# Kernel tuning notes

Hardware: AMD Instinct MI355X
Metric: run time of the kernel (lower is better)

The kernel has to match this reference:

```python
import jax, jax.numpy as jnp
import numpy as np

# Static per-expert capacities (tokens are laid out contiguously per expert)
CAPS = [1024, 512, 1024, 256, 1024, 512, 128, 1024, 512, 1024, 256, 512, 1024, 128, 64, 512]
TOTAL = sum(CAPS)  # 9536
E, H, I = 16, 1024, 4096
OFFSETS = np.concatenate([[0], np.cumsum(CAPS)])


def setup_inputs() -> dict:
    key = jax.random.key(0)
    ks = jax.random.split(key, 5)
    x = jax.random.normal(ks[0], (TOTAL, H), dtype=jnp.float32)
    W1 = jax.random.normal(ks[1], (E, I, H), dtype=jnp.float32) * 0.02
    b1 = jax.random.normal(ks[2], (E, I), dtype=jnp.float32) * 0.02
    W2 = jax.random.normal(ks[3], (E, H, I), dtype=jnp.float32) * 0.02
    b2 = jax.random.normal(ks[4], (E, H), dtype=jnp.float32) * 0.02
    return {"x": x, "W1": W1, "b1": b1, "W2": W2, "b2": b2}


def reference(x, W1, b1, W2, b2):
    # Grouped GEMM FFN: expert e processes rows [OFFSETS[e]:OFFSETS[e+1]]
    # out = gelu(x_e @ W1[e].T + b1[e]) @ W2[e].T + b2[e]
    outs = []
    for e in range(E):  # fixed, static loop over experts (capacities are static)
        xs = x[OFFSETS[e]:OFFSETS[e + 1]]                      # [cap_e, H]
        h = jax.nn.gelu(xs @ W1[e].T + b1[e], approximate=False)  # [cap_e, I]
        outs.append(h @ W2[e].T + b2[e])                       # [cap_e, H]
    return jnp.concatenate(outs, axis=0)                       # [TOTAL, H]
```

## Files before the change

kernel.cpp:

```cpp
#include <hip/hip_runtime.h>
#include <math.h>

typedef __attribute__((ext_vector_type(8))) short short8;
typedef __attribute__((ext_vector_type(4))) float f32x4;
typedef __attribute__((ext_vector_type(2))) unsigned int u32x2;

#define E_NUM 16
constexpr int CAPS[E_NUM] = {1024,512,1024,256,1024,512,128,1024,512,1024,256,512,1024,128,64,512};
constexpr int OFFS[E_NUM] = {0,1024,1536,2560,2816,3840,4352,4480,5504,6016,7040,7296,7808,8832,8960,9024};
constexpr int cdiv_(int a, int b){ return (a + b - 1) / b; }
constexpr int ilog2_(int v){ int l = 0; while ((1 << l) < v) ++l; return l; }

__device__ __forceinline__ unsigned int cvt_pk_bf16(float a, float b){
  unsigned int r;
  asm("v_cvt_pk_bf16_f32 %0, %1, %2" : "=v"(r) : "v"(a), "v"(b));
  return r;
}

template<bool A_BF16, bool GELU_OUT, int TM, int NDIM, int KDIM, int LOG_GN, int NWG>
__global__ __launch_bounds__(256, 4)
void expert_gemm(const void* __restrict__ Av, const float* __restrict__ W,
                 const float* __restrict__ bias, void* __restrict__ Outv)
{
  constexpr int STR  = 40;
  constexpr int A_SZ = TM * STR;
  constexpr int B_SZ = 128 * STR;
  constexpr int GN   = 1 << LOG_GN;
  constexpr int MFR  = TM / 32;
  static_assert(NWG % 8 == 0, "grid must be divisible by 8 for XCD swizzle");

  __shared__ __align__(16) unsigned short smem[2 * A_SZ + 2 * B_SZ];

  const int tid  = threadIdx.x;
  const int braw = blockIdx.x;
  const int t = (braw & 7) * (NWG / 8) + (braw >> 3);

  int m0 = 0, n0 = 0, Me = 0, tok0 = 0;
  size_t wbase = 0, bbase = 0;
  {
    int acc0 = 0;
    #pragma unroll
    for (int i = 0; i < E_NUM; ++i) {
      const int mt  = cdiv_(CAPS[i], TM);
      const int lmt = ilog2_(mt);
      const int nb  = mt * (NDIM / 128);
      if (t >= acc0 && t < acc0 + nb) {
        const int loc = t - acc0;
        const int g   = loc >> (lmt + LOG_GN);
        const int rem = loc & ((mt << LOG_GN) - 1);
        m0   = (rem >> LOG_GN) * TM;
        n0   = ((g << LOG_GN) | (rem & (GN - 1))) * 128;
        Me   = CAPS[i];
        tok0 = OFFS[i];
        wbase = (size_t)i * NDIM * KDIM;
        bbase = (size_t)i * NDIM;
      }
      acc0 += nb;
    }
  }
  const float* Wb = W + wbase;

  const int sr  = tid >> 3;
  const int skq = (tid & 7) * 4;
  const int hr  = tid >> 2;
  const int hc  = (tid & 3) * 8;

  const float*          Af = (const float*)Av;
  const unsigned short* Ah = (const unsigned short*)Av;

  f32x4 ra[4]; short8 ha[2]; f32x4 rb[4];

  auto load_tile = [&](int kt) {
    const int k0 = kt * 32;
    if constexpr (A_BF16) {
      #pragma unroll
      for (int i = 0; i < TM / 64; ++i)
        ha[i] = *reinterpret_cast<const short8*>(
            Ah + (size_t)(tok0 + m0 + hr + 64 * i) * KDIM + k0 + hc);
    } else {
      #pragma unroll
      for (int i = 0; i < TM / 32; ++i)
        ra[i] = *reinterpret_cast<const f32x4*>(
            Af + (size_t)(tok0 + m0 + sr + 32 * i) * KDIM + k0 + skq);
    }
    #pragma unroll
    for (int i = 0; i < 4; ++i)
      rb[i] = *reinterpret_cast<const f32x4*>(
          Wb + (size_t)(n0 + sr + 32 * i) * KDIM + k0 + skq);
  };

  auto write_tile = [&](int buf) {
    unsigned short* ab = smem + buf * A_SZ;
    unsigned short* bb = smem + 2 * A_SZ + buf * B_SZ;
    if constexpr (A_BF16) {
      #pragma unroll
      for (int i = 0; i < TM / 64; ++i)
        *reinterpret_cast<short8*>(ab + (hr + 64 * i) * STR + hc) = ha[i];
    } else {
      #pragma unroll
      for (int i = 0; i < TM / 32; ++i) {
        u32x2 p;
        p[0] = cvt_pk_bf16(ra[i][0], ra[i][1]);
        p[1] = cvt_pk_bf16(ra[i][2], ra[i][3]);
        *reinterpret_cast<u32x2*>(ab + (sr + 32 * i) * STR + skq) = p;
      }
    }
    #pragma unroll
    for (int i = 0; i < 4; ++i) {
      u32x2 p;
      p[0] = cvt_pk_bf16(rb[i][0], rb[i][1]);
      p[1] = cvt_pk_bf16(rb[i][2], rb[i][3]);
      *reinterpret_cast<u32x2*>(bb + (sr + 32 * i) * STR + skq) = p;
    }
  };

  const int lane = tid & 63;
  const int wv   = tid >> 6;
  const int wm   = (wv >> 1) * (TM / 2);
  const int wn   = (wv & 1) * 64;
  const int lrow = lane & 15;
  const int kcol = (lane >> 4) * 8;

  f32x4 acc_[MFR][4];
  #pragma unroll
  for (int i = 0; i < MFR; ++i)
    #pragma unroll
    for (int j = 0; j < 4; ++j)
      acc_[i][j] = (f32x4){0.f, 0.f, 0.f, 0.f};

  load_tile(0);
  write_tile(0);
  __syncthreads();

  constexpr int NT = KDIM / 32;
  for (int kt = 0; kt < NT; ++kt) {
    const int cur = kt & 1;
    if (kt + 1 < NT) load_tile(kt + 1);

    const unsigned short* ab = smem + cur * A_SZ;
    const unsigned short* bb = smem + 2 * A_SZ + cur * B_SZ;
    short8 afr[MFR], bfr[4];
    #pragma unroll
    for (int f = 0; f < MFR; ++f)
      afr[f] = *reinterpret_cast<const short8*>(ab + (wm + f * 16 + lrow) * STR + kcol);
    #pragma unroll
    for (int f = 0; f < 4; ++f)
      bfr[f] = *reinterpret_cast<const short8*>(bb + (wn + f * 16 + lrow) * STR + kcol);

    #pragma unroll
    for (int i = 0; i < MFR; ++i)
      #pragma unroll
      for (int j = 0; j < 4; ++j)
        acc_[i][j] = __builtin_amdgcn_mfma_f32_16x16x32_bf16(afr[i], bfr[j], acc_[i][j], 0, 0, 0);

    if (kt + 1 < NT) write_tile(cur ^ 1);
    __syncthreads();
  }

  float bv[4];
  #pragma unroll
  for (int f = 0; f < 4; ++f)
    bv[f] = bias[bbase + n0 + wn + f * 16 + lrow];

  if constexpr (GELU_OUT) {
    static_assert(TM == 128, "GELU path assumes 128-row tiles");
    unsigned short* hout = smem;
    #pragma unroll
    for (int i = 0; i < MFR; ++i) {
      const int rbase = wm + i * 16 + (lane >> 4) * 4;
      #pragma unroll
      for (int j = 0; j < 4; ++j) {
        #pragma unroll
        for (int jj = 0; jj < 4; ++jj) {
          float xv = acc_[i][j][jj] + bv[j];
          float g  = 0.5f * xv * (1.0f + erff(xv * 0.70710678118654752f));
          hout[(rbase + jj) * 128 + wn + j * 16 + lrow] = (unsigned short)(cvt_pk_bf16(g, g) & 0xFFFFu);
        }
      }
    }
    __syncthreads();
    unsigned short* Oh = (unsigned short*)Outv;
    #pragma unroll
    for (int it = 0; it < 8; ++it) {
      int row  = it * 16 + (tid >> 4);
      int c    = (tid & 15) * 8;
      int grow = m0 + row;
      if (grow < Me) {
        *reinterpret_cast<short8*>(Oh + (size_t)(tok0 + grow) * NDIM + n0 + c)
          = *reinterpret_cast<const short8*>(hout + row * 128 + c);
      }
    }
  } else {
    float* Of = (float*)Outv;
    #pragma unroll
    for (int i = 0; i < MFR; ++i) {
      const int rbase = wm + i * 16 + (lane >> 4) * 4;
      #pragma unroll
      for (int jj = 0; jj < 4; ++jj) {
        int grow = m0 + rbase + jj;
        if (grow < Me) {
          #pragma unroll
          for (int j = 0; j < 4; ++j) {
            Of[(size_t)(tok0 + grow) * NDIM + n0 + wn + j * 16 + lrow] = acc_[i][j][jj] + bv[j];
          }
        }
      }
    }
  }
}

extern "C" void kernel_launch(void* const* d_in, const int* in_sizes, int n_in,
                              void* d_out, int out_size, void* d_ws, size_t ws_size,
                              hipStream_t stream)
{
  const float* x  = (const float*)d_in[0];
  const float* W1 = (const float*)d_in[1];
  const float* b1 = (const float*)d_in[2];
  const float* W2 = (const float*)d_in[3];
  const float* b2 = (const float*)d_in[4];
  float* out = (float*)d_out;
  unsigned short* h = (unsigned short*)d_ws;

  expert_gemm<false, true, 128, 4096, 1024, 2, 75 * 32>
      <<<75 * 32, 256, 0, stream>>>((const void*)x, W1, b1, (void*)h);

  expert_gemm<true, false, 64, 1024, 4096, 1, 149 * 8>
      <<<149 * 8, 256, 0, stream>>>((const void*)h, W2, b2, (void*)out);
}
```

Before: 443.5 us.

## Stage A tiles via global_load_lds with XOR-swizzled LDS and pre-convert x to bf16

The A operand is now staged straight from global memory into LDS with global_load_lds, skipping the register round trip. The LDS padding (stride 40) is replaced by an XOR swizzle on dense 64-byte rows. A separate pass converts x to bf16 first so the first GEMM can use the same direct path, falling back when the workspace is too small. The second GEMM's group size also changes. This cuts register pressure and VGPR-to-LDS traffic, at the cost of an extra conversion kernel and launch, and it needs a larger workspace.

Result: faster. 398.2 us (-10.2%).

```diff
diff --git a/kernel.cpp b/kernel.cpp
--- a/kernel.cpp
+++ b/kernel.cpp
@@ -17,17 +17,39 @@
   return r;
 }
 
-template<bool A_BF16, bool GELU_OUT, int TM, int NDIM, int KDIM, int LOG_GN, int NWG>
+typedef __attribute__((address_space(1))) const unsigned char gas_u8;
+typedef __attribute__((address_space(3))) unsigned char las_u8;
+__device__ __forceinline__ void gl_lds16(const void* g, void* l){
+  __builtin_amdgcn_global_load_lds((gas_u8*)g, (las_u8*)l, 16, 0, 0);
+}
+
+__global__ __launch_bounds__(256) void cvt_bf16_kernel(const float* __restrict__ x,
+                                                       unsigned short* __restrict__ xb, int n8)
+{
+  int i = blockIdx.x * blockDim.x + threadIdx.x;
+  const int stride = gridDim.x * blockDim.x;
+  for (; i < n8; i += stride) {
+    f32x4 a = *reinterpret_cast<const f32x4*>(x + (size_t)i * 8);
+    f32x4 b = *reinterpret_cast<const f32x4*>(x + (size_t)i * 8 + 4);
+    u32x2 lo, hi;
+    lo[0] = cvt_pk_bf16(a[0], a[1]); lo[1] = cvt_pk_bf16(a[2], a[3]);
+    hi[0] = cvt_pk_bf16(b[0], b[1]); hi[1] = cvt_pk_bf16(b[2], b[3]);
+    *reinterpret_cast<u32x2*>(xb + (size_t)i * 8)     = lo;
+    *reinterpret_cast<u32x2*>(xb + (size_t)i * 8 + 4) = hi;
+  }
+}
+
+template<bool A_GLDS, bool GELU_OUT, int TM, int NDIM, int KDIM, int LOG_GN, int NWG>
 __global__ __launch_bounds__(256, 4)
 void expert_gemm(const void* __restrict__ Av, const float* __restrict__ W,
                  const float* __restrict__ bias, void* __restrict__ Outv)
 {
-  constexpr int STR  = 40;
-  constexpr int A_SZ = TM * STR;
-  constexpr int B_SZ = 128 * STR;
+  constexpr int A_SZ = TM * 32;
+  constexpr int B_SZ = 128 * 32;
   constexpr int GN   = 1 << LOG_GN;
   constexpr int MFR  = TM / 32;
   static_assert(NWG % 8 == 0, "grid must be divisible by 8 for XCD swizzle");
+  static_assert(!GELU_OUT || 2 * (A_SZ + B_SZ) >= 128 * 128, "GELU transpose needs 32KB");
 
   __shared__ __align__(16) unsigned short smem[2 * A_SZ + 2 * B_SZ];
 
@@ -60,66 +82,67 @@
   }
   const float* Wb = W + wbase;
 
-  const int sr  = tid >> 3;
-  const int skq = (tid & 7) * 4;
-  const int hr  = tid >> 2;
-  const int hc  = (tid & 3) * 8;
-
+  const int lane = tid & 63;
+  const int wv   = tid >> 6;
+  const int sr   = tid >> 3;
+  const int sc   = (tid & 7) * 8;
+  const int spc  = sc ^ ((sr & 3) << 4);
+
+  const unsigned short* Ah = (const unsigned short*)Av;
   const float*          Af = (const float*)Av;
-  const unsigned short* Ah = (const unsigned short*)Av;
-
-  f32x4 ra[4]; short8 ha[2]; f32x4 rb[4];
-
-  auto load_tile = [&](int kt) {
+
+  f32x4 ra[MFR]; f32x4 rb[4];
+
+  auto loadB = [&](int kt) {
     const int k0 = kt * 32;
-    if constexpr (A_BF16) {
-      #pragma unroll
-      for (int i = 0; i < TM / 64; ++i)
-        ha[i] = *reinterpret_cast<const short8*>(
-            Ah + (size_t)(tok0 + m0 + hr + 64 * i) * KDIM + k0 + hc);
-    } else {
-      #pragma unroll
-      for (int i = 0; i < TM / 32; ++i)
-        ra[i] = *reinterpret_cast<const f32x4*>(
-            Af + (size_t)(tok0 + m0 + sr + 32 * i) * KDIM + k0 + skq);
-    }
     #pragma unroll
     for (int i = 0; i < 4; ++i)
-      rb[i] = *reinterpret_cast<const f32x4*>(
-          Wb + (size_t)(n0 + sr + 32 * i) * KDIM + k0 + skq);
-  };
-
-  auto write_tile = [&](int buf) {
-    unsigned short* ab = smem + buf * A_SZ;
-    unsigned short* bb = smem + 2 * A_SZ + buf * B_SZ;
-    if constexpr (A_BF16) {
-      #pragma unroll
-      for (int i = 0; i < TM / 64; ++i)
-        *reinterpret_cast<short8*>(ab + (hr + 64 * i) * STR + hc) = ha[i];
-    } else {
-      #pragma unroll
-      for (int i = 0; i < TM / 32; ++i) {
-        u32x2 p;
-        p[0] = cvt_pk_bf16(ra[i][0], ra[i][1]);
-        p[1] = cvt_pk_bf16(ra[i][2], ra[i][3]);
-        *reinterpret_cast<u32x2*>(ab + (sr + 32 * i) * STR + skq) = p;
-      }
-    }
+      rb[i] = *reinterpret_cast<const f32x4*>(Wb + (size_t)(n0 + sr + 32 * i) * KDIM + k0 + (sc >> 1));
+  };
+  auto writeB = [&](int buf) {
+    char* bb = (char*)(smem + 2 * A_SZ + buf * B_SZ);
     #pragma unroll
     for (int i = 0; i < 4; ++i) {
       u32x2 p;
       p[0] = cvt_pk_bf16(rb[i][0], rb[i][1]);
       p[1] = cvt_pk_bf16(rb[i][2], rb[i][3]);
-      *reinterpret_cast<u32x2*>(bb + (sr + 32 * i) * STR + skq) = p;
-    }
-  };
-
-  const int lane = tid & 63;
-  const int wv   = tid >> 6;
+      *reinterpret_cast<u32x2*>(bb + (sr + 32 * i) * 64 + spc) = p;
+    }
+  };
+
+  auto stageA_glds = [&](int buf, int kt) {
+    constexpr int AI = TM / 64;
+    const unsigned short* Ag = Ah + (size_t)(tok0 + m0) * KDIM + kt * 32;
+    #pragma unroll
+    for (int j = 0; j < AI; ++j) {
+      const int rbase = wv * (AI * 16) + j * 16;
+      const int r     = rbase + (lane >> 2);
+      const int gblk  = (lane & 3) ^ (r & 3);
+      gl_lds16((const void*)(Ag + (size_t)r * KDIM + gblk * 8),
+               (void*)(smem + buf * A_SZ + rbase * 32));
+    }
+  };
+  auto loadA_reg = [&](int kt) {
+    const int k0 = kt * 32;
+    #pragma unroll
+    for (int i = 0; i < MFR; ++i)
+      ra[i] = *reinterpret_cast<const f32x4*>(Af + (size_t)(tok0 + m0 + sr + 32 * i) * KDIM + k0 + (sc >> 1));
+  };
+  auto writeA_reg = [&](int buf) {
+    char* ab = (char*)(smem + buf * A_SZ);
+    #pragma unroll
+    for (int i = 0; i < MFR; ++i) {
+      u32x2 p;
+      p[0] = cvt_pk_bf16(ra[i][0], ra[i][1]);
+      p[1] = cvt_pk_bf16(ra[i][2], ra[i][3]);
+      *reinterpret_cast<u32x2*>(ab + (sr + 32 * i) * 64 + spc) = p;
+    }
+  };
+
   const int wm   = (wv >> 1) * (TM / 2);
   const int wn   = (wv & 1) * 64;
   const int lrow = lane & 15;
-  const int kcol = (lane >> 4) * 8;
+  const int fcs  = ((lane >> 4) << 4) ^ ((lane & 3) << 4);
 
   f32x4 acc_[MFR][4];
   #pragma unroll
@@ -128,24 +151,29 @@
     for (int j = 0; j < 4; ++j)
       acc_[i][j] = (f32x4){0.f, 0.f, 0.f, 0.f};
 
-  load_tile(0);
-  write_tile(0);
+  loadB(0);
+  if constexpr (A_GLDS) stageA_glds(0, 0); else { loadA_reg(0); writeA_reg(0); }
+  writeB(0);
   __syncthreads();
 
   constexpr int NT = KDIM / 32;
   for (int kt = 0; kt < NT; ++kt) {
     const int cur = kt & 1;
-    if (kt + 1 < NT) load_tile(kt + 1);
-
-    const unsigned short* ab = smem + cur * A_SZ;
-    const unsigned short* bb = smem + 2 * A_SZ + cur * B_SZ;
+    if (kt + 1 < NT) {
+      loadB(kt + 1);
+      if constexpr (A_GLDS) stageA_glds(cur ^ 1, kt + 1);
+      else                  loadA_reg(kt + 1);
+    }
+
+    const char* ab = (const char*)(smem + cur * A_SZ);
+    const char* bb = (const char*)(smem + 2 * A_SZ + cur * B_SZ);
     short8 afr[MFR], bfr[4];
     #pragma unroll
     for (int f = 0; f < MFR; ++f)
-      afr[f] = *reinterpret_cast<const short8*>(ab + (wm + f * 16 + lrow) * STR + kcol);
+      afr[f] = *reinterpret_cast<const short8*>(ab + (wm + f * 16 + lrow) * 64 + fcs);
     #pragma unroll
     for (int f = 0; f < 4; ++f)
-      bfr[f] = *reinterpret_cast<const short8*>(bb + (wn + f * 16 + lrow) * STR + kcol);
+      bfr[f] = *reinterpret_cast<const short8*>(bb + (wn + f * 16 + lrow) * 64 + fcs);
 
     #pragma unroll
     for (int i = 0; i < MFR; ++i)
@@ -153,7 +181,10 @@
       for (int j = 0; j < 4; ++j)
         acc_[i][j] = __builtin_amdgcn_mfma_f32_16x16x32_bf16(afr[i], bfr[j], acc_[i][j], 0, 0, 0);
 
-    if (kt + 1 < NT) write_tile(cur ^ 1);
+    if (kt + 1 < NT) {
+      writeB(cur ^ 1);
+      if constexpr (!A_GLDS) writeA_reg(cur ^ 1);
+    }
     __syncthreads();
   }
 
@@ -219,11 +250,23 @@
   const float* W2 = (const float*)d_in[3];
   const float* b2 = (const float*)d_in[4];
   float* out = (float*)d_out;
-  unsigned short* h = (unsigned short*)d_ws;
-
-  expert_gemm<false, true, 128, 4096, 1024, 2, 75 * 32>
-      <<<75 * 32, 256, 0, stream>>>((const void*)x, W1, b1, (void*)h);
-
-  expert_gemm<true, false, 64, 1024, 4096, 1, 149 * 8>
+
+  constexpr size_t H_BYTES  = (size_t)9536 * 4096 * 2;
+  constexpr size_t XB_BYTES = (size_t)9536 * 1024 * 2;
+  unsigned short* h  = (unsigned short*)d_ws;
+  unsigned short* xb = (unsigned short*)((char*)d_ws + H_BYTES);
+
+  const bool use_xb = ws_size >= H_BYTES + XB_BYTES;
+
+  if (use_xb) {
+    cvt_bf16_kernel<<<2048, 256, 0, stream>>>(x, xb, 9536 * 1024 / 8);
+    expert_gemm<true, true, 128, 4096, 1024, 2, 75 * 32>
+        <<<75 * 32, 256, 0, stream>>>((const void*)xb, W1, b1, (void*)h);
+  } else {
+    expert_gemm<false, true, 128, 4096, 1024, 2, 75 * 32>
+        <<<75 * 32, 256, 0, stream>>>((const void*)x, W1, b1, (void*)h);
+  }
+
+  expert_gemm<true, false, 64, 1024, 4096, 0, 149 * 8>
       <<<149 * 8, 256, 0, stream>>>((const void*)h, W2, b2, (void*)out);
 }
```
